# Kernel optimization log

Measured on AMD Instinct MI355X. Metric: run time of the kernel, lower is better.

Reference implementation:

```python
import jax, jax.numpy as jnp
import numpy as np

NUM_CAPSULE = 32
DIM_CAPSULE = 16
ROUTINGS = 3
EPS = 1e-7  # K.epsilon()


def squash(x, axis=-1):
    s2 = jnp.sum(jnp.square(x), axis=axis, keepdims=True) + EPS
    scale = jnp.sqrt(s2) / (0.5 + s2)
    return scale * x


def setup_inputs() -> dict:
    key = jax.random.key(0)
    kx, kw = jax.random.split(key)
    x = jax.random.normal(kx, (128, 2048, 128), dtype=jnp.float32)
    # glorot-uniform-scale init for (in_dim, num_capsule*dim_capsule)
    fan_in, fan_out = 128, NUM_CAPSULE * DIM_CAPSULE
    limit = np.sqrt(6.0 / (fan_in + fan_out)).astype(np.float32)
    kernel = jax.random.uniform(kw, (fan_in, fan_out), dtype=jnp.float32,
                                minval=-limit, maxval=limit)
    return {"x": x, "kernel": kernel}


def reference(x, kernel):
    B, N, _ = x.shape
    # share_weights=True: 1x1 conv1d == matmul over input_dim_capsule
    hat = jnp.einsum('bnd,dm->bnm', x, kernel)            # (B, N, C*D)
    hat = hat.reshape(B, N, NUM_CAPSULE, DIM_CAPSULE)
    hat = jnp.transpose(hat, (0, 2, 1, 3))                # (B, C, N, D)
    b = jnp.zeros(hat.shape[:3], dtype=hat.dtype)         # (B, C, N)
    o = None
    for i in range(ROUTINGS):
        c = jax.nn.softmax(b, axis=1)                     # softmax over output capsules
        o = squash(jnp.einsum('bcn,bcnd->bcd', c, hat))   # (B, C, D)
        if i < ROUTINGS - 1:
            b = jnp.einsum('bcd,bcnd->bcn', o, hat)       # agreement (replaces b, per code)
    return o
```

## Files before the change

kernel.cpp:

```cpp
#include <hip/hip_runtime.h>
#include <hip/hip_bf16.h>


#define SEQ 2048
#define KD  128

typedef __attribute__((ext_vector_type(8))) short bf16x8;
typedef __attribute__((ext_vector_type(4))) float f32x4;

__device__ __forceinline__ short f2bf(float f) {
  unsigned u = __float_as_uint(f);
  u = u + 0x7fffu + ((u >> 16) & 1u);
  return (short)(u >> 16);
}
__device__ __forceinline__ int swz(int row) {
  return ((row & 7) << 4) ^ ((row & 24) << 2);
}

__global__ __launch_bounds__(256) void prep_k(const float* __restrict__ x,
                                              short* __restrict__ xs,
                                              float* __restrict__ Sp) {
  int blk = blockIdx.x;
  int t = threadIdx.x, oct = t & 15, rsub = t >> 4;
  size_t row0 = (size_t)blk * 128;
  char* dst = (char*)xs + (size_t)blk * 32768;
  float sac[8] = {0.f,0.f,0.f,0.f,0.f,0.f,0.f,0.f};
  #pragma unroll
  for (int sub = 0; sub < 8; ++sub) {
    int r = sub * 16 + rsub;
    const float* gp = x + (row0 + r) * KD + oct * 8;
    float4 f0 = *(const float4*)gp, f1 = *(const float4*)(gp + 4);
    bf16x8 v; short* vp = (short*)&v;
    vp[0] = f2bf(f0.x); vp[1] = f2bf(f0.y); vp[2] = f2bf(f0.z); vp[3] = f2bf(f0.w);
    vp[4] = f2bf(f1.x); vp[5] = f2bf(f1.y); vp[6] = f2bf(f1.z); vp[7] = f2bf(f1.w);
    sac[0] += f0.x; sac[1] += f0.y; sac[2] += f0.z; sac[3] += f0.w;
    sac[4] += f1.x; sac[5] += f1.y; sac[6] += f1.z; sac[7] += f1.w;
    *(bf16x8*)(dst + ((r * 256 + oct * 16) ^ swz(r))) = v;
  }
  __shared__ float red[2048];
  float4* rp = (float4*)&red[rsub * 128 + oct * 8];
  rp[0] = make_float4(sac[0], sac[1], sac[2], sac[3]);
  rp[1] = make_float4(sac[4], sac[5], sac[6], sac[7]);
  __syncthreads();
  if (t < 128) {
    float s = 0.f;
    #pragma unroll
    for (int i = 0; i < 16; ++i) s += red[i * 128 + t];
    Sp[blk * KD + t] = s;
  }
}

__global__ __launch_bounds__(256, 2) void pass_k(const short* __restrict__ xs,
                                                 const float* __restrict__ W,
                                                 const float* __restrict__ Sp,
                                                 const float* __restrict__ ypin,
                                                 float* __restrict__ yout,
                                                 int iter0) {
  __shared__ char ldsbuf[49152];
  char* lx  = ldsbuf;
  char* lw  = ldsbuf + 32768;
  char* lcn = ldsbuf + 40960;
  float* yv   = (float*)ldsbuf;
  float* sarr = (float*)(ldsbuf + 16384);
  float* olds = (float*)(ldsbuf + 18432);
  float* yred = (float*)ldsbuf;

  int b = blockIdx.x >> 2;
  int t = threadIdx.x;
  int wv = t >> 6, lane = t & 63, l15 = lane & 15, lg = lane >> 4;

  if (iter0) {
    if (t < 128) {
      float s = 0.f;
      #pragma unroll
      for (int j = 0; j < 16; ++j) s += Sp[(b * 16 + j) * KD + t];
      sarr[t] = s * (1.f / 32.f);
    }
    __syncthreads();
    #pragma unroll
    for (int i = 0; i < 16; ++i) { int idx = i * 256 + t; yv[idx] = sarr[idx & 127]; }
  } else {
    const float* y0 = ypin + (size_t)b * 4 * 4096;
    #pragma unroll
    for (int i = 0; i < 16; ++i) {
      int idx = i * 256 + t;
      yv[idx] = y0[idx] + y0[4096 + idx] + y0[8192 + idx] + y0[12288 + idx];
    }
  }
  __syncthreads();
  float sreg[2];
  #pragma unroll
  for (int h = 0; h < 2; ++h) {
    int cd = h * 256 + t, c = cd >> 4, d = cd & 15;
    float acc = 0.f;
    #pragma unroll 8
    for (int k = 0; k < KD; ++k) acc += yv[c * KD + k] * W[k * 512 + c * 16 + d];
    sreg[h] = acc;
  }
  __syncthreads();
  sarr[t] = sreg[0]; sarr[256 + t] = sreg[1];
  __syncthreads();
  #pragma unroll
  for (int h = 0; h < 2; ++h) {
    int cd = h * 256 + t, c = cd >> 4;
    float s2 = 1e-7f;
    #pragma unroll
    for (int dd = 0; dd < 16; ++dd) { float v = sarr[c * 16 + dd]; s2 += v * v; }
    olds[cd] = (sqrtf(s2) / (0.5f + s2)) * sreg[h];
  }
  __syncthreads();
  #pragma unroll
  for (int i = 0; i < 16; ++i) {
    int idx = i * 256 + t, c = idx >> 7, k = idx & 127;
    float acc = 0.f;
    #pragma unroll
    for (int dd = 0; dd < 16; ++dd) acc += olds[c * 16 + dd] * W[k * 512 + c * 16 + dd];
    *(short*)(lw + ((c * 256 + k * 2) ^ ((c & 7) << 4))) = f2bf(acc);
  }
  __syncthreads();

  f32x4 zz = {0.f, 0.f, 0.f, 0.f};
  f32x4 yacc[2][8];
  #pragma unroll
  for (int i = 0; i < 2; ++i)
    #pragma unroll
    for (int j = 0; j < 8; ++j) yacc[i][j] = zz;

  for (int chunk = 0; chunk < 4; ++chunk) {
    {
      const char* gs = (const char*)xs + ((size_t)blockIdx.x * 4 + chunk) * 32768;
      #pragma unroll
      for (int sub = 0; sub < 8; ++sub) {
        int off = sub * 4096 + t * 16;
        *(bf16x8*)(lx + off) = *(const bf16x8*)(gs + off);
      }
    }
    __syncthreads();

    f32x4 sc[2][2];
    sc[0][0] = zz; sc[0][1] = zz; sc[1][0] = zz; sc[1][1] = zz;
    #pragma unroll
    for (int ks = 0; ks < 4; ++ks) {
      bf16x8 a[2], bw[2];
      #pragma unroll
      for (int mi = 0; mi < 2; ++mi) {
        int row = wv * 32 + mi * 16 + l15;
        a[mi] = *(const bf16x8*)(lx + ((row * 256 + ks * 64 + lg * 16) ^ swz(row)));
      }
      #pragma unroll
      for (int ct = 0; ct < 2; ++ct) {
        int cc = ct * 16 + l15;
        bw[ct] = *(const bf16x8*)(lw + ((cc * 256 + ks * 64 + lg * 16) ^ ((cc & 7) << 4)));
      }
      #pragma unroll
      for (int mi = 0; mi < 2; ++mi)
        #pragma unroll
        for (int ct = 0; ct < 2; ++ct)
          sc[mi][ct] = __builtin_amdgcn_mfma_f32_16x16x32_bf16(a[mi], bw[ct], sc[mi][ct], 0, 0, 0);
    }

    #pragma unroll
    for (int mi = 0; mi < 2; ++mi) {
      #pragma unroll
      for (int r = 0; r < 4; ++r) {
        float v0 = sc[mi][0][r], v1 = sc[mi][1][r];
        float mx = fmaxf(v0, v1);
        mx = fmaxf(mx, __shfl_xor(mx, 1));
        mx = fmaxf(mx, __shfl_xor(mx, 2));
        mx = fmaxf(mx, __shfl_xor(mx, 4));
        mx = fmaxf(mx, __shfl_xor(mx, 8));
        float e0 = __expf(v0 - mx), e1 = __expf(v1 - mx);
        float sm = e0 + e1;
        sm += __shfl_xor(sm, 1); sm += __shfl_xor(sm, 2);
        sm += __shfl_xor(sm, 4); sm += __shfl_xor(sm, 8);
        float inv = 1.f / sm;
        int row = wv * 32 + mi * 16 + lg * 4 + r;
        int c0 = l15, c1 = 16 + l15;
        *(short*)(lcn + ((c0 * 256 + row * 2) ^ ((c0 & 7) << 4))) = f2bf(e0 * inv);
        *(short*)(lcn + ((c1 * 256 + row * 2) ^ ((c1 & 7) << 4))) = f2bf(e1 * inv);
      }
    }
    __syncthreads();

    {
      bf16x8 a2[2];
      #pragma unroll
      for (int m2 = 0; m2 < 2; ++m2) {
        int cc = m2 * 16 + l15;
        a2[m2] = *(const bf16x8*)(lcn + ((cc * 256 + wv * 64 + lg * 16) ^ ((cc & 7) << 4)));
      }
      #pragma unroll
      for (int nt = 0; nt < 8; ++nt) {
        bf16x8 bx;
        short* bp = (short*)&bx;
        int col = nt * 16 + l15;
        int rbase = wv * 32 + lg * 8;
        #pragma unroll
        for (int j = 0; j < 8; ++j) {
          int row = rbase + j;
          bp[j] = *(const short*)(lx + ((row * 256 + col * 2) ^ swz(row)));
        }
        yacc[0][nt] = __builtin_amdgcn_mfma_f32_16x16x32_bf16(a2[0], bx, yacc[0][nt], 0, 0, 0);
        yacc[1][nt] = __builtin_amdgcn_mfma_f32_16x16x32_bf16(a2[1], bx, yacc[1][nt], 0, 0, 0);
      }
    }
    __syncthreads();
  }

  #pragma unroll 1
  for (int round = 0; round < 4; ++round) {
    if (wv == round) {
      #pragma unroll
      for (int m2 = 0; m2 < 2; ++m2)
        #pragma unroll
        for (int nt = 0; nt < 8; ++nt)
          #pragma unroll
          for (int r = 0; r < 4; ++r) {
            int cc = m2 * 16 + lg * 4 + r;
            int kk = nt * 16 + l15;
            if (round == 0) yred[cc * 128 + kk]  = yacc[m2][nt][r];
            else            yred[cc * 128 + kk] += yacc[m2][nt][r];
          }
    }
    __syncthreads();
  }
  float* yo = yout + (size_t)blockIdx.x * 4096;
  #pragma unroll
  for (int i = 0; i < 16; ++i) yo[i * 256 + t] = yred[i * 256 + t];
}

__global__ __launch_bounds__(64) void out_k(const float* __restrict__ W,
                                            const float* __restrict__ yp,
                                            float* __restrict__ out) {
  int b = blockIdx.x >> 5, c = blockIdx.x & 31;
  int l = threadIdx.x, d = l & 15, kg = l >> 4;
  const float* Wc = W + c * 16;
  const float* y0 = yp + (size_t)b * 4 * 4096 + c * KD;
  float s = 0.f;
  #pragma unroll 8
  for (int i = 0; i < 32; ++i) {
    int k = kg * 32 + i;
    float yvv = y0[k] + y0[4096 + k] + y0[8192 + k] + y0[12288 + k];
    s += yvv * Wc[k * 512 + d];
  }
  s += __shfl_xor(s, 16); s += __shfl_xor(s, 32);
  float s2 = s * s;
  s2 += __shfl_xor(s2, 1); s2 += __shfl_xor(s2, 2);
  s2 += __shfl_xor(s2, 4); s2 += __shfl_xor(s2, 8);
  s2 += 1e-7f;
  float o = (sqrtf(s2) / (0.5f + s2)) * s;
  if (l < 16) out[(size_t)b * 512 + c * 16 + l] = o;
}

extern "C" void kernel_launch(void* const* d_in, const int* in_sizes, int n_in,
                              void* d_out, int out_size, void* d_ws, size_t ws_size,
                              hipStream_t stream) {
  const float* x = (const float*)d_in[0];
  const float* W = (const float*)d_in[1];
  float* out = (float*)d_out;
  char* ws = (char*)d_ws;
  float* Sp = (float*)ws;
  float* y1 = (float*)(ws + (1u << 20));
  float* y2 = (float*)(ws + 9u * (1u << 20));
  short* xs = (short*)(ws + 17u * (1u << 20));

  prep_k<<<dim3(2048), dim3(256), 0, stream>>>(x, xs, Sp);
  pass_k<<<dim3(512), dim3(256), 0, stream>>>(xs, W, Sp, nullptr, y1, 1);
  pass_k<<<dim3(512), dim3(256), 0, stream>>>(xs, W, nullptr, y1, y2, 0);
  out_k <<<dim3(4096), dim3(64), 0, stream>>>(W, y2, out);
}
```

Measured before the change: 332.3 us.

## Fuse both routing passes and output squash into one per-batch kernel

```diff
diff --git a/kernel.cpp b/kernel.cpp
--- a/kernel.cpp
+++ b/kernel.cpp
@@ -50,206 +50,192 @@
   }
 }
 
-__global__ __launch_bounds__(256, 2) void pass_k(const short* __restrict__ xs,
-                                                 const float* __restrict__ W,
-                                                 const float* __restrict__ Sp,
-                                                 const float* __restrict__ ypin,
-                                                 float* __restrict__ yout,
-                                                 int iter0) {
-  __shared__ char ldsbuf[49152];
-  char* lx  = ldsbuf;
-  char* lw  = ldsbuf + 32768;
-  char* lcn = ldsbuf + 40960;
+__global__ __launch_bounds__(512, 1) void route_k(const short* __restrict__ xs,
+                                                  const float* __restrict__ W,
+                                                  const float* __restrict__ Sp,
+                                                  float* __restrict__ out) {
+  __shared__ char ldsbuf[90112];
+  int b = blockIdx.x;
+  int t = threadIdx.x;
+  int wv = t >> 6, tm = wv >> 2, w4 = wv & 3;
+  int lane = t & 63, l15 = lane & 15, lg = lane >> 4;
+  int tt = t & 255;
+
+  char* lx  = ldsbuf + tm * 40960;
+  char* lcn = ldsbuf + tm * 40960 + 32768;
+  char* lw  = ldsbuf + 81920;
   float* yv   = (float*)ldsbuf;
   float* sarr = (float*)(ldsbuf + 16384);
   float* olds = (float*)(ldsbuf + 18432);
-  float* yred = (float*)ldsbuf;
-
-  int b = blockIdx.x >> 2;
-  int t = threadIdx.x;
-  int wv = t >> 6, lane = t & 63, l15 = lane & 15, lg = lane >> 4;
-
-  if (iter0) {
-    if (t < 128) {
-      float s = 0.f;
-      #pragma unroll
-      for (int j = 0; j < 16; ++j) s += Sp[(b * 16 + j) * KD + t];
-      sarr[t] = s * (1.f / 32.f);
-    }
+
+  f32x4 zz = {0.f, 0.f, 0.f, 0.f};
+
+  for (int iter = 0; iter < 2; ++iter) {
+    if (iter == 0) {
+      if (t < 128) {
+        float s = 0.f;
+        #pragma unroll
+        for (int j = 0; j < 16; ++j) s += Sp[(b * 16 + j) * KD + t];
+        sarr[t] = s * (1.f / 32.f);
+      }
+      __syncthreads();
+      #pragma unroll
+      for (int i = 0; i < 8; ++i) { int idx = i * 512 + t; yv[idx] = sarr[idx & 127]; }
+      __syncthreads();
+    }
+
+    float sreg;
+    {
+      int c = t >> 4, d = t & 15;
+      float acc = 0.f;
+      #pragma unroll 8
+      for (int k = 0; k < KD; ++k) acc += yv[c * KD + k] * W[k * 512 + c * 16 + d];
+      sreg = acc;
+    }
+    sarr[t] = sreg;
     __syncthreads();
-    #pragma unroll
-    for (int i = 0; i < 16; ++i) { int idx = i * 256 + t; yv[idx] = sarr[idx & 127]; }
-  } else {
-    const float* y0 = ypin + (size_t)b * 4 * 4096;
-    #pragma unroll
-    for (int i = 0; i < 16; ++i) {
-      int idx = i * 256 + t;
-      yv[idx] = y0[idx] + y0[4096 + idx] + y0[8192 + idx] + y0[12288 + idx];
-    }
-  }
-  __syncthreads();
-  float sreg[2];
-  #pragma unroll
-  for (int h = 0; h < 2; ++h) {
-    int cd = h * 256 + t, c = cd >> 4, d = cd & 15;
+    {
+      int c = t >> 4;
+      float s2 = 1e-7f;
+      #pragma unroll
+      for (int dd = 0; dd < 16; ++dd) { float v = sarr[c * 16 + dd]; s2 += v * v; }
+      olds[t] = (sqrtf(s2) / (0.5f + s2)) * sreg;
+    }
+    __syncthreads();
+    #pragma unroll
+    for (int i = 0; i < 8; ++i) {
+      int idx = i * 512 + t, c = idx >> 7, k = idx & 127;
+      float acc = 0.f;
+      #pragma unroll
+      for (int dd = 0; dd < 16; ++dd) acc += olds[c * 16 + dd] * W[k * 512 + c * 16 + dd];
+      *(short*)(lw + ((c * 256 + k * 2) ^ ((c & 7) << 4))) = f2bf(acc);
+    }
+    __syncthreads();
+
+    f32x4 yacc[2][8];
+    #pragma unroll
+    for (int i = 0; i < 2; ++i)
+      #pragma unroll
+      for (int j = 0; j < 8; ++j) yacc[i][j] = zz;
+
+    for (int step = 0; step < 8; ++step) {
+      {
+        int ch = step * 2 + tm;
+        const char* gs = (const char*)xs + ((size_t)b * 16 + ch) * 32768;
+        #pragma unroll
+        for (int sub = 0; sub < 8; ++sub) {
+          int off = sub * 4096 + tt * 16;
+          *(bf16x8*)(lx + off) = *(const bf16x8*)(gs + off);
+        }
+      }
+      __syncthreads();
+
+      f32x4 sc[2][2];
+      sc[0][0] = zz; sc[0][1] = zz; sc[1][0] = zz; sc[1][1] = zz;
+      #pragma unroll
+      for (int ks = 0; ks < 4; ++ks) {
+        bf16x8 a[2], bw[2];
+        #pragma unroll
+        for (int mi = 0; mi < 2; ++mi) {
+          int row = w4 * 32 + mi * 16 + l15;
+          a[mi] = *(const bf16x8*)(lx + ((row * 256 + ks * 64 + lg * 16) ^ swz(row)));
+        }
+        #pragma unroll
+        for (int ct = 0; ct < 2; ++ct) {
+          int cc = ct * 16 + l15;
+          bw[ct] = *(const bf16x8*)(lw + ((cc * 256 + ks * 64 + lg * 16) ^ ((cc & 7) << 4)));
+        }
+        #pragma unroll
+        for (int mi = 0; mi < 2; ++mi)
+          #pragma unroll
+          for (int ct = 0; ct < 2; ++ct)
+            sc[mi][ct] = __builtin_amdgcn_mfma_f32_16x16x32_bf16(a[mi], bw[ct], sc[mi][ct], 0, 0, 0);
+      }
+
+      #pragma unroll
+      for (int mi = 0; mi < 2; ++mi) {
+        #pragma unroll
+        for (int r = 0; r < 4; ++r) {
+          float v0 = sc[mi][0][r], v1 = sc[mi][1][r];
+          float mx = fmaxf(v0, v1);
+          mx = fmaxf(mx, __shfl_xor(mx, 1));
+          mx = fmaxf(mx, __shfl_xor(mx, 2));
+          mx = fmaxf(mx, __shfl_xor(mx, 4));
+          mx = fmaxf(mx, __shfl_xor(mx, 8));
+          float e0 = __expf(v0 - mx), e1 = __expf(v1 - mx);
+          float sm = e0 + e1;
+          sm += __shfl_xor(sm, 1); sm += __shfl_xor(sm, 2);
+          sm += __shfl_xor(sm, 4); sm += __shfl_xor(sm, 8);
+          float inv = 1.f / sm;
+          int row = w4 * 32 + mi * 16 + lg * 4 + r;
+          int c0 = l15, c1 = 16 + l15;
+          *(short*)(lcn + ((c0 * 256 + row * 2) ^ ((c0 & 7) << 4))) = f2bf(e0 * inv);
+          *(short*)(lcn + ((c1 * 256 + row * 2) ^ ((c1 & 7) << 4))) = f2bf(e1 * inv);
+        }
+      }
+      __syncthreads();
+
+      {
+        bf16x8 a2[2];
+        #pragma unroll
+        for (int m2 = 0; m2 < 2; ++m2) {
+          int cc = m2 * 16 + l15;
+          a2[m2] = *(const bf16x8*)(lcn + ((cc * 256 + w4 * 64 + lg * 16) ^ ((cc & 7) << 4)));
+        }
+        #pragma unroll
+        for (int nt = 0; nt < 8; ++nt) {
+          bf16x8 bx;
+          short* bp = (short*)&bx;
+          int col = nt * 16 + l15;
+          int rbase = w4 * 32 + lg * 8;
+          #pragma unroll
+          for (int j = 0; j < 8; ++j) {
+            int row = rbase + j;
+            bp[j] = *(const short*)(lx + ((row * 256 + col * 2) ^ swz(row)));
+          }
+          yacc[0][nt] = __builtin_amdgcn_mfma_f32_16x16x32_bf16(a2[0], bx, yacc[0][nt], 0, 0, 0);
+          yacc[1][nt] = __builtin_amdgcn_mfma_f32_16x16x32_bf16(a2[1], bx, yacc[1][nt], 0, 0, 0);
+        }
+      }
+      __syncthreads();
+    }
+
+    #pragma unroll 1
+    for (int round = 0; round < 8; ++round) {
+      if (wv == round) {
+        #pragma unroll
+        for (int m2 = 0; m2 < 2; ++m2)
+          #pragma unroll
+          for (int nt = 0; nt < 8; ++nt)
+            #pragma unroll
+            for (int r = 0; r < 4; ++r) {
+              int cc = m2 * 16 + lg * 4 + r;
+              int kk = nt * 16 + l15;
+              if (round == 0) yv[cc * 128 + kk]  = yacc[m2][nt][r];
+              else            yv[cc * 128 + kk] += yacc[m2][nt][r];
+            }
+      }
+      __syncthreads();
+    }
+  }
+
+  float sreg;
+  {
+    int c = t >> 4, d = t & 15;
     float acc = 0.f;
     #pragma unroll 8
     for (int k = 0; k < KD; ++k) acc += yv[c * KD + k] * W[k * 512 + c * 16 + d];
-    sreg[h] = acc;
-  }
+    sreg = acc;
+  }
+  sarr[t] = sreg;
   __syncthreads();
-  sarr[t] = sreg[0]; sarr[256 + t] = sreg[1];
-  __syncthreads();
-  #pragma unroll
-  for (int h = 0; h < 2; ++h) {
-    int cd = h * 256 + t, c = cd >> 4;
+  {
+    int c = t >> 4;
     float s2 = 1e-7f;
     #pragma unroll
     for (int dd = 0; dd < 16; ++dd) { float v = sarr[c * 16 + dd]; s2 += v * v; }
-    olds[cd] = (sqrtf(s2) / (0.5f + s2)) * sreg[h];
-  }
-  __syncthreads();
-  #pragma unroll
-  for (int i = 0; i < 16; ++i) {
-    int idx = i * 256 + t, c = idx >> 7, k = idx & 127;
-    float acc = 0.f;
-    #pragma unroll
-    for (int dd = 0; dd < 16; ++dd) acc += olds[c * 16 + dd] * W[k * 512 + c * 16 + dd];
-    *(short*)(lw + ((c * 256 + k * 2) ^ ((c & 7) << 4))) = f2bf(acc);
-  }
-  __syncthreads();
-
-  f32x4 zz = {0.f, 0.f, 0.f, 0.f};
-  f32x4 yacc[2][8];
-  #pragma unroll
-  for (int i = 0; i < 2; ++i)
-    #pragma unroll
-    for (int j = 0; j < 8; ++j) yacc[i][j] = zz;
-
-  for (int chunk = 0; chunk < 4; ++chunk) {
-    {
-      const char* gs = (const char*)xs + ((size_t)blockIdx.x * 4 + chunk) * 32768;
-      #pragma unroll
-      for (int sub = 0; sub < 8; ++sub) {
-        int off = sub * 4096 + t * 16;
-        *(bf16x8*)(lx + off) = *(const bf16x8*)(gs + off);
-      }
-    }
-    __syncthreads();
-
-    f32x4 sc[2][2];
-    sc[0][0] = zz; sc[0][1] = zz; sc[1][0] = zz; sc[1][1] = zz;
-    #pragma unroll
-    for (int ks = 0; ks < 4; ++ks) {
-      bf16x8 a[2], bw[2];
-      #pragma unroll
-      for (int mi = 0; mi < 2; ++mi) {
-        int row = wv * 32 + mi * 16 + l15;
-        a[mi] = *(const bf16x8*)(lx + ((row * 256 + ks * 64 + lg * 16) ^ swz(row)));
-      }
-      #pragma unroll
-      for (int ct = 0; ct < 2; ++ct) {
-        int cc = ct * 16 + l15;
-        bw[ct] = *(const bf16x8*)(lw + ((cc * 256 + ks * 64 + lg * 16) ^ ((cc & 7) << 4)));
-      }
-      #pragma unroll
-      for (int mi = 0; mi < 2; ++mi)
-        #pragma unroll
-        for (int ct = 0; ct < 2; ++ct)
-          sc[mi][ct] = __builtin_amdgcn_mfma_f32_16x16x32_bf16(a[mi], bw[ct], sc[mi][ct], 0, 0, 0);
-    }
-
-    #pragma unroll
-    for (int mi = 0; mi < 2; ++mi) {
-      #pragma unroll
-      for (int r = 0; r < 4; ++r) {
-        float v0 = sc[mi][0][r], v1 = sc[mi][1][r];
-        float mx = fmaxf(v0, v1);
-        mx = fmaxf(mx, __shfl_xor(mx, 1));
-        mx = fmaxf(mx, __shfl_xor(mx, 2));
-        mx = fmaxf(mx, __shfl_xor(mx, 4));
-        mx = fmaxf(mx, __shfl_xor(mx, 8));
-        float e0 = __expf(v0 - mx), e1 = __expf(v1 - mx);
-        float sm = e0 + e1;
-        sm += __shfl_xor(sm, 1); sm += __shfl_xor(sm, 2);
-        sm += __shfl_xor(sm, 4); sm += __shfl_xor(sm, 8);
-        float inv = 1.f / sm;
-        int row = wv * 32 + mi * 16 + lg * 4 + r;
-        int c0 = l15, c1 = 16 + l15;
-        *(short*)(lcn + ((c0 * 256 + row * 2) ^ ((c0 & 7) << 4))) = f2bf(e0 * inv);
-        *(short*)(lcn + ((c1 * 256 + row * 2) ^ ((c1 & 7) << 4))) = f2bf(e1 * inv);
-      }
-    }
-    __syncthreads();
-
-    {
-      bf16x8 a2[2];
-      #pragma unroll
-      for (int m2 = 0; m2 < 2; ++m2) {
-        int cc = m2 * 16 + l15;
-        a2[m2] = *(const bf16x8*)(lcn + ((cc * 256 + wv * 64 + lg * 16) ^ ((cc & 7) << 4)));
-      }
-      #pragma unroll
-      for (int nt = 0; nt < 8; ++nt) {
-        bf16x8 bx;
-        short* bp = (short*)&bx;
-        int col = nt * 16 + l15;
-        int rbase = wv * 32 + lg * 8;
-        #pragma unroll
-        for (int j = 0; j < 8; ++j) {
-          int row = rbase + j;
-          bp[j] = *(const short*)(lx + ((row * 256 + col * 2) ^ swz(row)));
-        }
-        yacc[0][nt] = __builtin_amdgcn_mfma_f32_16x16x32_bf16(a2[0], bx, yacc[0][nt], 0, 0, 0);
-        yacc[1][nt] = __builtin_amdgcn_mfma_f32_16x16x32_bf16(a2[1], bx, yacc[1][nt], 0, 0, 0);
-      }
-    }
-    __syncthreads();
-  }
-
-  #pragma unroll 1
-  for (int round = 0; round < 4; ++round) {
-    if (wv == round) {
-      #pragma unroll
-      for (int m2 = 0; m2 < 2; ++m2)
-        #pragma unroll
-        for (int nt = 0; nt < 8; ++nt)
-          #pragma unroll
-          for (int r = 0; r < 4; ++r) {
-            int cc = m2 * 16 + lg * 4 + r;
-            int kk = nt * 16 + l15;
-            if (round == 0) yred[cc * 128 + kk]  = yacc[m2][nt][r];
-            else            yred[cc * 128 + kk] += yacc[m2][nt][r];
-          }
-    }
-    __syncthreads();
-  }
-  float* yo = yout + (size_t)blockIdx.x * 4096;
-  #pragma unroll
-  for (int i = 0; i < 16; ++i) yo[i * 256 + t] = yred[i * 256 + t];
-}
-
-__global__ __launch_bounds__(64) void out_k(const float* __restrict__ W,
-                                            const float* __restrict__ yp,
-                                            float* __restrict__ out) {
-  int b = blockIdx.x >> 5, c = blockIdx.x & 31;
-  int l = threadIdx.x, d = l & 15, kg = l >> 4;
-  const float* Wc = W + c * 16;
-  const float* y0 = yp + (size_t)b * 4 * 4096 + c * KD;
-  float s = 0.f;
-  #pragma unroll 8
-  for (int i = 0; i < 32; ++i) {
-    int k = kg * 32 + i;
-    float yvv = y0[k] + y0[4096 + k] + y0[8192 + k] + y0[12288 + k];
-    s += yvv * Wc[k * 512 + d];
-  }
-  s += __shfl_xor(s, 16); s += __shfl_xor(s, 32);
-  float s2 = s * s;
-  s2 += __shfl_xor(s2, 1); s2 += __shfl_xor(s2, 2);
-  s2 += __shfl_xor(s2, 4); s2 += __shfl_xor(s2, 8);
-  s2 += 1e-7f;
-  float o = (sqrtf(s2) / (0.5f + s2)) * s;
-  if (l < 16) out[(size_t)b * 512 + c * 16 + l] = o;
+    out[(size_t)b * 512 + t] = (sqrtf(s2) / (0.5f + s2)) * sreg;
+  }
 }
 
 extern "C" void kernel_launch(void* const* d_in, const int* in_sizes, int n_in,
@@ -260,12 +246,8 @@
   float* out = (float*)d_out;
   char* ws = (char*)d_ws;
   float* Sp = (float*)ws;
-  float* y1 = (float*)(ws + (1u << 20));
-  float* y2 = (float*)(ws + 9u * (1u << 20));
-  short* xs = (short*)(ws + 17u * (1u << 20));
-
-  prep_k<<<dim3(2048), dim3(256), 0, stream>>>(x, xs, Sp);
-  pass_k<<<dim3(512), dim3(256), 0, stream>>>(xs, W, Sp, nullptr, y1, 1);
-  pass_k<<<dim3(512), dim3(256), 0, stream>>>(xs, W, nullptr, y1, y2, 0);
-  out_k <<<dim3(4096), dim3(64), 0, stream>>>(W, y2, out);
-}
+  short* xs = (short*)(ws + (1u << 20));
+
+  prep_k <<<dim3(2048), dim3(256), 0, stream>>>(x, xs, Sp);
+  route_k<<<dim3(128),  dim3(512), 0, stream>>>(xs, W, Sp, out);
+}
```

Result: slower. 442.5 us (+33.1%).
